# Performance work log

Measured on AMD Instinct MI355X. Metric: run time of the kernel, lower is better.

The kernel has to match this reference:

```python
import jax, jax.numpy as jnp
import numpy as np

SIZE_IN = 4096
SIZE_OUT = 4096
COEF = 8


def _make_mask(size_in, size_out, coef):
    # block-diagonal canceler: output row block i sees input column block i
    inp_sec = size_in // coef
    out_sec = size_out // coef
    row_block = np.arange(size_out) // out_sec  # [size_out]
    col_block = np.arange(size_in) // inp_sec   # [size_in]
    return (row_block[:, None] == col_block[None, :]).astype(np.float32)


def setup_inputs() -> dict:
    key = jax.random.key(0)
    kx, kw, kb = jax.random.split(key, 3)
    x = jax.random.normal(kx, (16384, SIZE_IN), dtype=jnp.float32)
    # kaiming_uniform_(a=sqrt(5)) on [size_out, size_in]: bound = sqrt(6/((1+5)*fan_in)) = 1/sqrt(fan_in)
    bound_w = 1.0 / np.sqrt(SIZE_IN)
    weights = jax.random.uniform(kw, (SIZE_OUT, SIZE_IN), minval=-bound_w, maxval=bound_w, dtype=jnp.float32)
    bound_b = 1.0 / np.sqrt(SIZE_IN)
    bias = jax.random.uniform(kb, (SIZE_OUT,), minval=-bound_b, maxval=bound_b, dtype=jnp.float32)
    mask = jnp.asarray(_make_mask(SIZE_IN, SIZE_OUT, COEF))
    return {"x": x, "weights": weights, "bias": bias, "mask": mask}


def reference(x, weights, bias, mask):
    # faithful to torch: full dense GEMM on the masked weight
    w = weights * mask                      # [size_out, size_in]
    return x @ w.T + bias                   # [batch, size_out]
```

## Files before the change

### kernel.cpp

```cpp
#include <hip/hip_runtime.h>
#include <hip/hip_bf16.h>


typedef __bf16 bf16x8 __attribute__((ext_vector_type(8)));
typedef float  f32x4  __attribute__((ext_vector_type(4)));

constexpr int LD = 4096;

__device__ __forceinline__ bf16x8 cvt8(f32x4 u, f32x4 v) {
    bf16x8 p;
    p[0] = (__bf16)u[0]; p[1] = (__bf16)u[1]; p[2] = (__bf16)u[2]; p[3] = (__bf16)u[3];
    p[4] = (__bf16)v[0]; p[5] = (__bf16)v[1]; p[6] = (__bf16)v[2]; p[7] = (__bf16)v[3];
    return p;
}

__device__ __forceinline__ void gload32(f32x4& q0, f32x4& q1, const void* p) {
    asm volatile("global_load_dwordx4 %0, %2, off\n\t"
                 "global_load_dwordx4 %1, %2, off offset:16"
                 : "=&v"(q0), "=&v"(q1)
                 : "v"(p));
}

__global__ __launch_bounds__(256)
void pack_w(const float* __restrict__ w, __bf16* __restrict__ wt)
{
    const int g = blockIdx.x * 256 + threadIdx.x;
    const int base = g * 16;
    const int o = base >> 9;
    const int k = base & 511;
    const float* src = w + (size_t)o * LD + ((o >> 9) << 9) + k;
    f32x4 a = *(const f32x4*)(src);
    f32x4 b = *(const f32x4*)(src + 4);
    f32x4 c = *(const f32x4*)(src + 8);
    f32x4 d = *(const f32x4*)(src + 12);
    *(bf16x8*)(wt + base)     = cvt8(a, b);
    *(bf16x8*)(wt + base + 8) = cvt8(c, d);
}

__global__ __launch_bounds__(512, 4)
void fc_gemm(const float* __restrict__ x, const __bf16* __restrict__ wt,
             const float* __restrict__ bias, float* __restrict__ out)
{
    __shared__ __align__(16) char smem[81920];

    const int tid  = threadIdx.x;
    const int lane = tid & 63;
    const int wid  = tid >> 6;
    const int wm   = wid >> 2;
    const int wn   = wid & 3;

    const int bid  = blockIdx.x;
    const int xcd  = bid & 7;
    const int slot = bid >> 3;
    const int gm   = slot >> 1;
    const int nh   = slot & 1;
    const int koff = xcd << 9;

    const int trA = tid >> 3;
    const int qA  = tid & 7;
    const int soA = trA * 128 + ((qA * 16) ^ ((trA & 7) << 4));
    const float* xs = x + (size_t)(gm * 64 + trA) * LD + koff + qA * 8;

    const int trB = tid >> 1;
    const int hB  = tid & 1;
    const int swB = (trB & 7) << 4;
    int soB[4];
#pragma unroll
    for (int s = 0; s < 4; ++s)
        soB[s] = trB * 128 + ((hB * 64 + s * 16) ^ swB);
    const __bf16* bs = wt + (size_t)(xcd * 512 + nh * 256 + trB) * 512 + hB * 32;

    f32x4 stA[2][2];
    f32x4 stB[2][2][2];

    f32x4 acc[2][4];
#pragma unroll
    for (int i = 0; i < 2; ++i)
#pragma unroll
        for (int n = 0; n < 4; ++n)
            acc[i][n] = {0.f, 0.f, 0.f, 0.f};

    auto issueTile = [&](int kt, int set) {
        gload32(stB[set][0][0], stB[set][0][1], bs + kt * 64);
        gload32(stB[set][1][0], stB[set][1][1], bs + kt * 64 + 16);
        gload32(stA[set][0], stA[set][1], xs + kt * 64);
    };
    auto storeTile = [&](int set, int buf) {
        char* ab = smem + buf * 8192;
        char* bb = smem + 16384 + buf * 32768;
        *(bf16x8*)(ab + soA) = cvt8(stA[set][0], stA[set][1]);
        *(f32x4*)(bb + soB[0]) = stB[set][0][0];
        *(f32x4*)(bb + soB[1]) = stB[set][0][1];
        *(f32x4*)(bb + soB[2]) = stB[set][1][0];
        *(f32x4*)(bb + soB[3]) = stB[set][1][1];
    };

    issueTile(0, 0);
    issueTile(1, 1);
    asm volatile("s_waitcnt vmcnt(6)" ::: "memory");
    __builtin_amdgcn_sched_barrier(0);
    storeTile(0, 0);
    asm volatile("s_waitcnt lgkmcnt(0)" ::: "memory");
    __builtin_amdgcn_s_barrier();

    const int arow = lane & 15;
    const int ag   = lane >> 4;
    const int fswz = (arow & 7) << 4;
    const int aRowBase = (wm * 32 + arow) * 128;
    const int bRowBase = (wn * 64 + arow) * 128;

#pragma unroll
    for (int kt = 0; kt < 8; ++kt) {
        const int cur = kt & 1;
        if (kt < 6) issueTile(kt + 2, cur);

        const char* aB = smem + cur * 8192;
        const char* bB = smem + 16384 + cur * 32768;
#pragma unroll
        for (int kk = 0; kk < 2; ++kk) {
            const int kx = (kk * 64 + ag * 16) ^ fswz;
            bf16x8 av[2], bv[4];
#pragma unroll
            for (int mf = 0; mf < 2; ++mf)
                av[mf] = *(const bf16x8*)(aB + aRowBase + mf * 2048 + kx);
#pragma unroll
            for (int nf = 0; nf < 4; ++nf)
                bv[nf] = *(const bf16x8*)(bB + bRowBase + nf * 2048 + kx);
#pragma unroll
            for (int mf = 0; mf < 2; ++mf)
#pragma unroll
                for (int nf = 0; nf < 4; ++nf)
                    acc[mf][nf] = __builtin_amdgcn_mfma_f32_16x16x32_bf16(
                        av[mf], bv[nf], acc[mf][nf], 0, 0, 0);
        }

        if (kt < 7) {
            if (kt < 6) { asm volatile("s_waitcnt vmcnt(6)" ::: "memory"); }
            else        { asm volatile("s_waitcnt vmcnt(0)" ::: "memory"); }
            __builtin_amdgcn_sched_barrier(0);
            storeTile(cur ^ 1, cur ^ 1);
            asm volatile("s_waitcnt lgkmcnt(0)" ::: "memory");
            __builtin_amdgcn_s_barrier();
        }
    }

    __syncthreads();

    float* pw = (float*)(smem) + wid * 1280;
    const int r0 = ag * 4;
    const int colbase = xcd * 512 + nh * 256 + wn * 64;
    const int rowg    = gm * 64 + wm * 32;
    float bv4[4];
#pragma unroll
    for (int nf = 0; nf < 4; ++nf)
        bv4[nf] = bias[colbase + nf * 16 + arow];

#pragma unroll
    for (int mf = 0; mf < 2; ++mf) {
#pragma unroll
        for (int nf = 0; nf < 4; ++nf)
#pragma unroll
            for (int r2 = 0; r2 < 4; ++r2) {
                const int lr  = r0 + r2;
                const int col = (nf * 16 + arow) ^ ((lr & 12) << 2);
                pw[lr * 80 + col] = acc[mf][nf][r2] + bv4[nf];
            }
#pragma unroll
        for (int p = 0; p < 4; ++p) {
            const int q  = p * 64 + lane;
            const int lr = q >> 4;
            const int ci = q & 15;
            const f32x4 v4 = *(const f32x4*)(pw + lr * 80 + 4 * (ci ^ (lr & 12)));
            __builtin_nontemporal_store(v4,
                (f32x4*)(out + (size_t)(rowg + mf * 16 + lr) * LD + colbase + ci * 4));
        }
    }
}

extern "C" void kernel_launch(void* const* d_in, const int* in_sizes, int n_in,
                              void* d_out, int out_size, void* d_ws, size_t ws_size,
                              hipStream_t stream)
{
    const float* x    = (const float*)d_in[0];
    const float* wgt  = (const float*)d_in[1];
    const float* bias = (const float*)d_in[2];
    float* out = (float*)d_out;
    __bf16* wt = (__bf16*)d_ws;

    pack_w<<<dim3(512), dim3(256), 0, stream>>>(wgt, wt);
    fc_gemm<<<dim3(4096), dim3(512), 0, stream>>>(x, wt, bias, out);
}
```

Measured before the change: 150.5 us.

## Double M tile to 128 rows and switch to 32x32x16 MFMA

Each block now covers 128 rows of x instead of 64, which halves the grid and the redundant reloads of the packed weight tile per block. The inner loop uses 32x32x16 bf16 MFMA with 64x64 warp tiles instead of 16x16x32 with 32x64, so each LDS fragment read feeds more FLOPs. Shared memory grows to 96KB and the occupancy hint of 4 blocks is dropped, so fewer blocks fit per CU. The epilogue is reworked for the 32x32 accumulator layout.

```diff
diff --git a/kernel.cpp b/kernel.cpp
--- a/kernel.cpp
+++ b/kernel.cpp
@@ -4,6 +4,7 @@
 
 typedef __bf16 bf16x8 __attribute__((ext_vector_type(8)));
 typedef float  f32x4  __attribute__((ext_vector_type(4)));
+typedef float  f32x16 __attribute__((ext_vector_type(16)));
 
 constexpr int LD = 4096;
 
@@ -37,11 +38,11 @@
     *(bf16x8*)(wt + base + 8) = cvt8(c, d);
 }
 
-__global__ __launch_bounds__(512, 4)
+__global__ __launch_bounds__(512)
 void fc_gemm(const float* __restrict__ x, const __bf16* __restrict__ wt,
              const float* __restrict__ bias, float* __restrict__ out)
 {
-    __shared__ __align__(16) char smem[81920];
+    __shared__ __align__(16) char smem[98304];
 
     const int tid  = threadIdx.x;
     const int lane = tid & 63;
@@ -55,11 +56,14 @@
     const int gm   = slot >> 1;
     const int nh   = slot & 1;
     const int koff = xcd << 9;
+    const int colbase = xcd * 512 + nh * 256;
 
-    const int trA = tid >> 3;
-    const int qA  = tid & 7;
-    const int soA = trA * 128 + ((qA * 16) ^ ((trA & 7) << 4));
-    const float* xs = x + (size_t)(gm * 64 + trA) * LD + koff + qA * 8;
+    const int trA = tid >> 2;
+    const int qA  = tid & 3;
+    const int swA = (trA & 7) << 4;
+    const int soA0 = trA * 128 + ((qA * 32)      ^ swA);
+    const int soA1 = trA * 128 + ((qA * 32 + 16) ^ swA);
+    const float* xs = x + (size_t)(gm * 128 + trA) * LD + koff + qA * 16;
 
     const int trB = tid >> 1;
     const int hB  = tid & 1;
@@ -68,74 +72,76 @@
 #pragma unroll
     for (int s = 0; s < 4; ++s)
         soB[s] = trB * 128 + ((hB * 64 + s * 16) ^ swB);
-    const __bf16* bs = wt + (size_t)(xcd * 512 + nh * 256 + trB) * 512 + hB * 32;
+    const __bf16* bs = wt + (size_t)(colbase + trB) * 512 + hB * 32;
 
-    f32x4 stA[2][2];
-    f32x4 stB[2][2][2];
+    f32x4 stA[2][4];
+    f32x4 stB[2][4];
 
-    f32x4 acc[2][4];
+    f32x16 acc[2][2];
 #pragma unroll
     for (int i = 0; i < 2; ++i)
 #pragma unroll
-        for (int n = 0; n < 4; ++n)
-            acc[i][n] = {0.f, 0.f, 0.f, 0.f};
+        for (int n = 0; n < 2; ++n)
+            acc[i][n] = {0.f};
 
     auto issueTile = [&](int kt, int set) {
-        gload32(stB[set][0][0], stB[set][0][1], bs + kt * 64);
-        gload32(stB[set][1][0], stB[set][1][1], bs + kt * 64 + 16);
+        gload32(stB[set][0], stB[set][1], bs + kt * 64);
+        gload32(stB[set][2], stB[set][3], bs + kt * 64 + 16);
         gload32(stA[set][0], stA[set][1], xs + kt * 64);
+        gload32(stA[set][2], stA[set][3], xs + kt * 64 + 8);
     };
     auto storeTile = [&](int set, int buf) {
-        char* ab = smem + buf * 8192;
-        char* bb = smem + 16384 + buf * 32768;
-        *(bf16x8*)(ab + soA) = cvt8(stA[set][0], stA[set][1]);
-        *(f32x4*)(bb + soB[0]) = stB[set][0][0];
-        *(f32x4*)(bb + soB[1]) = stB[set][0][1];
-        *(f32x4*)(bb + soB[2]) = stB[set][1][0];
-        *(f32x4*)(bb + soB[3]) = stB[set][1][1];
+        char* ab = smem + buf * 16384;
+        char* bb = smem + 32768 + buf * 32768;
+        *(bf16x8*)(ab + soA0) = cvt8(stA[set][0], stA[set][1]);
+        *(bf16x8*)(ab + soA1) = cvt8(stA[set][2], stA[set][3]);
+        *(f32x4*)(bb + soB[0]) = stB[set][0];
+        *(f32x4*)(bb + soB[1]) = stB[set][1];
+        *(f32x4*)(bb + soB[2]) = stB[set][2];
+        *(f32x4*)(bb + soB[3]) = stB[set][3];
     };
 
     issueTile(0, 0);
     issueTile(1, 1);
-    asm volatile("s_waitcnt vmcnt(6)" ::: "memory");
+    asm volatile("s_waitcnt vmcnt(8)" ::: "memory");
     __builtin_amdgcn_sched_barrier(0);
     storeTile(0, 0);
     asm volatile("s_waitcnt lgkmcnt(0)" ::: "memory");
     __builtin_amdgcn_s_barrier();
 
-    const int arow = lane & 15;
-    const int ag   = lane >> 4;
-    const int fswz = (arow & 7) << 4;
-    const int aRowBase = (wm * 32 + arow) * 128;
-    const int bRowBase = (wn * 64 + arow) * 128;
+    const int r32 = lane & 31;
+    const int hi  = lane >> 5;
+    const int arow0 = wm * 64 + r32;
+    const int brow0 = wn * 64 + r32;
+    const int aoff0 = arow0 * 128, aoff1 = (arow0 + 32) * 128;
+    const int boff0 = brow0 * 128, boff1 = (brow0 + 32) * 128;
+    const int aswz0 = (arow0 & 7) << 4;
+    const int bswz0 = (brow0 & 7) << 4;
 
 #pragma unroll
     for (int kt = 0; kt < 8; ++kt) {
         const int cur = kt & 1;
         if (kt < 6) issueTile(kt + 2, cur);
 
-        const char* aB = smem + cur * 8192;
-        const char* bB = smem + 16384 + cur * 32768;
+        const char* aB = smem + cur * 16384;
+        const char* bB = smem + 32768 + cur * 32768;
 #pragma unroll
-        for (int kk = 0; kk < 2; ++kk) {
-            const int kx = (kk * 64 + ag * 16) ^ fswz;
-            bf16x8 av[2], bv[4];
-#pragma unroll
-            for (int mf = 0; mf < 2; ++mf)
-                av[mf] = *(const bf16x8*)(aB + aRowBase + mf * 2048 + kx);
-#pragma unroll
-            for (int nf = 0; nf < 4; ++nf)
-                bv[nf] = *(const bf16x8*)(bB + bRowBase + nf * 2048 + kx);
-#pragma unroll
-            for (int mf = 0; mf < 2; ++mf)
-#pragma unroll
-                for (int nf = 0; nf < 4; ++nf)
-                    acc[mf][nf] = __builtin_amdgcn_mfma_f32_16x16x32_bf16(
-                        av[mf], bv[nf], acc[mf][nf], 0, 0, 0);
+        for (int ks = 0; ks < 4; ++ks) {
+            const int ka = (ks * 32 + hi * 16) ^ aswz0;
+            const int kb = (ks * 32 + hi * 16) ^ bswz0;
+            bf16x8 av[2], bv[2];
+            av[0] = *(const bf16x8*)(aB + aoff0 + ka);
+            av[1] = *(const bf16x8*)(aB + aoff1 + ka);
+            bv[0] = *(const bf16x8*)(bB + boff0 + kb);
+            bv[1] = *(const bf16x8*)(bB + boff1 + kb);
+            acc[0][0] = __builtin_amdgcn_mfma_f32_32x32x16_bf16(av[0], bv[0], acc[0][0], 0, 0, 0);
+            acc[0][1] = __builtin_amdgcn_mfma_f32_32x32x16_bf16(av[0], bv[1], acc[0][1], 0, 0, 0);
+            acc[1][0] = __builtin_amdgcn_mfma_f32_32x32x16_bf16(av[1], bv[0], acc[1][0], 0, 0, 0);
+            acc[1][1] = __builtin_amdgcn_mfma_f32_32x32x16_bf16(av[1], bv[1], acc[1][1], 0, 0, 0);
         }
 
         if (kt < 7) {
-            if (kt < 6) { asm volatile("s_waitcnt vmcnt(6)" ::: "memory"); }
+            if (kt < 6) { asm volatile("s_waitcnt vmcnt(8)" ::: "memory"); }
             else        { asm volatile("s_waitcnt vmcnt(0)" ::: "memory"); }
             __builtin_amdgcn_sched_barrier(0);
             storeTile(cur ^ 1, cur ^ 1);
@@ -146,33 +152,31 @@
 
     __syncthreads();
 
-    float* pw = (float*)(smem) + wid * 1280;
-    const int r0 = ag * 4;
-    const int colbase = xcd * 512 + nh * 256 + wn * 64;
-    const int rowg    = gm * 64 + wm * 32;
-    float bv4[4];
+    float* pw = (float*)smem + wid * 2560;
+    float bv2[2];
 #pragma unroll
-    for (int nf = 0; nf < 4; ++nf)
-        bv4[nf] = bias[colbase + nf * 16 + arow];
+    for (int ni = 0; ni < 2; ++ni)
+        bv2[ni] = bias[colbase + wn * 64 + ni * 32 + r32];
 
 #pragma unroll
-    for (int mf = 0; mf < 2; ++mf) {
+    for (int mi = 0; mi < 2; ++mi) {
 #pragma unroll
-        for (int nf = 0; nf < 4; ++nf)
+        for (int ni = 0; ni < 2; ++ni)
 #pragma unroll
-            for (int r2 = 0; r2 < 4; ++r2) {
-                const int lr  = r0 + r2;
-                const int col = (nf * 16 + arow) ^ ((lr & 12) << 2);
-                pw[lr * 80 + col] = acc[mf][nf][r2] + bv4[nf];
+            for (int r = 0; r < 16; ++r) {
+                const int row = (r & 3) + 8 * (r >> 2) + 4 * hi;
+                const int col = (ni * 32 + r32) ^ ((row & 12) << 2);
+                pw[row * 80 + col] = acc[mi][ni][r] + bv2[ni];
             }
 #pragma unroll
-        for (int p = 0; p < 4; ++p) {
+        for (int p = 0; p < 8; ++p) {
             const int q  = p * 64 + lane;
             const int lr = q >> 4;
             const int ci = q & 15;
             const f32x4 v4 = *(const f32x4*)(pw + lr * 80 + 4 * (ci ^ (lr & 12)));
             __builtin_nontemporal_store(v4,
-                (f32x4*)(out + (size_t)(rowg + mf * 16 + lr) * LD + colbase + ci * 4));
+                (f32x4*)(out + (size_t)(gm * 128 + wm * 64 + mi * 32 + lr) * LD
+                         + colbase + wn * 64 + ci * 4));
         }
     }
 }
@@ -188,5 +192,5 @@
     __bf16* wt = (__bf16*)d_ws;
 
     pack_w<<<dim3(512), dim3(256), 0, stream>>>(wgt, wt);
-    fc_gemm<<<dim3(4096), dim3(512), 0, stream>>>(x, wt, bias, out);
+    fc_gemm<<<dim3(2048), dim3(512), 0, stream>>>(x, wt, bias, out);
 }
```

Result: no change. 149.3 us (-0.8%).

## Enlarge GEMM tile to 256x256 with finer-grained interleaved load/MFMA pipeline

Applied to the files above, without the earlier changes.

Each block now computes a 256-row by 256-column output tile instead of 64x256, cutting the grid from 4096 to 1024 blocks. The larger tile lets each loaded weight tile be reused across more rows, reducing redundant global and LDS traffic. The main loop becomes a hand-scheduled ping-pong pipeline where global loads, LDS writes, fragment reads and MFMA bursts are interleaved at half-tile granularity, with barriers and s_setprio around the MFMA groups. In exchange, LDS grows to 128KB and accumulator registers grow fourfold, so occupancy drops to 2 blocks per CU and fewer blocks are available to hide latency.

```diff
diff --git a/kernel.cpp b/kernel.cpp
--- a/kernel.cpp
+++ b/kernel.cpp
@@ -14,11 +14,18 @@
     return p;
 }
 
-__device__ __forceinline__ void gload32(f32x4& q0, f32x4& q1, const void* p) {
+__device__ __forceinline__ void gload64(f32x4& a, f32x4& b, f32x4& c, f32x4& d,
+                                        const void* p) {
+    asm volatile("global_load_dwordx4 %0, %4, off\n\t"
+                 "global_load_dwordx4 %1, %4, off offset:16\n\t"
+                 "global_load_dwordx4 %2, %4, off offset:32\n\t"
+                 "global_load_dwordx4 %3, %4, off offset:48"
+                 : "=&v"(a), "=&v"(b), "=&v"(c), "=&v"(d) : "v"(p));
+}
+__device__ __forceinline__ void gload32(f32x4& a, f32x4& b, const void* p) {
     asm volatile("global_load_dwordx4 %0, %2, off\n\t"
                  "global_load_dwordx4 %1, %2, off offset:16"
-                 : "=&v"(q0), "=&v"(q1)
-                 : "v"(p));
+                 : "=&v"(a), "=&v"(b) : "v"(p));
 }
 
 __global__ __launch_bounds__(256)
@@ -37,11 +44,50 @@
     *(bf16x8*)(wt + base + 8) = cvt8(c, d);
 }
 
-__global__ __launch_bounds__(512, 4)
+#define VMW(N)                                                    \
+    do {                                                          \
+        asm volatile("s_waitcnt vmcnt(" #N ")" ::: "memory");     \
+        __builtin_amdgcn_sched_barrier(0);                        \
+    } while (0)
+
+#define RD(TH, MH, KK)                                                        \
+    do {                                                                      \
+        const char* aB_ = smem + (TH) * 32768;                                \
+        const char* bB_ = smem + 65536 + (TH) * 32768;                        \
+        _Pragma("unroll")                                                     \
+        for (int f = 0; f < 4; ++f) {                                         \
+            const int row = wm * 128 + (MH) * 64 + f * 16 + arow;             \
+            av[f] = *(const bf16x8*)(aB_ + row * 128 +                        \
+                        (((KK) * 64 + ag * 16) ^ ((row & 7) << 4)));          \
+        }                                                                     \
+        _Pragma("unroll")                                                     \
+        for (int n = 0; n < 4; ++n) {                                         \
+            const int row = wn * 64 + n * 16 + arow;                          \
+            bv[n] = *(const bf16x8*)(bB_ + row * 128 +                        \
+                        (((KK) * 64 + ag * 16) ^ ((row & 7) << 4)));          \
+        }                                                                     \
+    } while (0)
+
+#define FIRE(MH)                                                              \
+    do {                                                                      \
+        __builtin_amdgcn_s_barrier();                                         \
+        asm volatile("s_waitcnt lgkmcnt(0)" ::: "memory");                    \
+        __builtin_amdgcn_s_setprio(1);                                        \
+        _Pragma("unroll")                                                     \
+        for (int f = 0; f < 4; ++f)                                           \
+            _Pragma("unroll")                                                 \
+            for (int n = 0; n < 4; ++n)                                       \
+                acc[(MH) * 4 + f][n] = __builtin_amdgcn_mfma_f32_16x16x32_bf16( \
+                    av[f], bv[n], acc[(MH) * 4 + f][n], 0, 0, 0);             \
+        __builtin_amdgcn_s_setprio(0);                                        \
+        __builtin_amdgcn_s_barrier();                                         \
+    } while (0)
+
+__global__ __launch_bounds__(512, 2)
 void fc_gemm(const float* __restrict__ x, const __bf16* __restrict__ wt,
              const float* __restrict__ bias, float* __restrict__ out)
 {
-    __shared__ __align__(16) char smem[81920];
+    __shared__ __align__(16) char smem[131072];
 
     const int tid  = threadIdx.x;
     const int lane = tid & 63;
@@ -50,120 +96,101 @@
     const int wn   = wid & 3;
 
     const int bid  = blockIdx.x;
-    const int xcd  = bid & 7;
+    const int j    = bid & 7;
     const int slot = bid >> 3;
     const int gm   = slot >> 1;
-    const int nh   = slot & 1;
-    const int koff = xcd << 9;
-
-    const int trA = tid >> 3;
-    const int qA  = tid & 7;
-    const int soA = trA * 128 + ((qA * 16) ^ ((trA & 7) << 4));
-    const float* xs = x + (size_t)(gm * 64 + trA) * LD + koff + qA * 8;
-
-    const int trB = tid >> 1;
-    const int hB  = tid & 1;
-    const int swB = (trB & 7) << 4;
-    int soB[4];
-#pragma unroll
-    for (int s = 0; s < 4; ++s)
-        soB[s] = trB * 128 + ((hB * 64 + s * 16) ^ swB);
-    const __bf16* bs = wt + (size_t)(xcd * 512 + nh * 256 + trB) * 512 + hB * 32;
-
-    f32x4 stA[2][2];
-    f32x4 stB[2][2][2];
-
-    f32x4 acc[2][4];
-#pragma unroll
-    for (int i = 0; i < 2; ++i)
+    const int gh   = slot & 1;
+    const int koff    = j << 9;
+    const int colbase = (j << 9) + (gh << 8);
+
+    const int sRow = tid >> 2;
+    const int sQ   = tid & 3;
+    const int swzS = (sRow & 7) << 4;
+    const int soA0 = sRow * 128 + ((sQ * 32)      ^ swzS);
+    const int soA1 = sRow * 128 + ((sQ * 32 + 16) ^ swzS);
+    const float*  xsB = x  + ((size_t)gm * 256 + sRow) * LD + koff + sQ * 16;
+    const __bf16* wtB = wt + ((size_t)colbase + sRow) * 512 + sQ * 16;
+
+    f32x4 stA[2][4];
+    f32x4 stB[2][2];
+
+    f32x4 acc[8][4];
+#pragma unroll
+    for (int i = 0; i < 8; ++i)
 #pragma unroll
         for (int n = 0; n < 4; ++n)
             acc[i][n] = {0.f, 0.f, 0.f, 0.f};
 
-    auto issueTile = [&](int kt, int set) {
-        gload32(stB[set][0][0], stB[set][0][1], bs + kt * 64);
-        gload32(stB[set][1][0], stB[set][1][1], bs + kt * 64 + 16);
-        gload32(stA[set][0], stA[set][1], xs + kt * 64);
-    };
-    auto storeTile = [&](int set, int buf) {
-        char* ab = smem + buf * 8192;
-        char* bb = smem + 16384 + buf * 32768;
-        *(bf16x8*)(ab + soA) = cvt8(stA[set][0], stA[set][1]);
-        *(f32x4*)(bb + soB[0]) = stB[set][0][0];
-        *(f32x4*)(bb + soB[1]) = stB[set][0][1];
-        *(f32x4*)(bb + soB[2]) = stB[set][1][0];
-        *(f32x4*)(bb + soB[3]) = stB[set][1][1];
-    };
-
-    issueTile(0, 0);
-    issueTile(1, 1);
-    asm volatile("s_waitcnt vmcnt(6)" ::: "memory");
-    __builtin_amdgcn_sched_barrier(0);
-    storeTile(0, 0);
+    auto issueA = [&](int kt, int h) {
+        gload64(stA[h][0], stA[h][1], stA[h][2], stA[h][3],
+                xsB + (size_t)h * 128 * LD + kt * 64);
+    };
+    auto issueB = [&](int kt, int h) {
+        gload32(stB[h][0], stB[h][1], wtB + (size_t)h * 65536 + kt * 64);
+    };
+    auto writeA = [&](int kt, int h) {
+        char* base = smem + (kt & 1) * 32768 + h * 16384;
+        *(bf16x8*)(base + soA0) = cvt8(stA[h][0], stA[h][1]);
+        *(bf16x8*)(base + soA1) = cvt8(stA[h][2], stA[h][3]);
+    };
+    auto writeB = [&](int kt, int h) {
+        char* base = smem + 65536 + (kt & 1) * 32768 + h * 16384;
+        *(f32x4*)(base + soA0) = stB[h][0];
+        *(f32x4*)(base + soA1) = stB[h][1];
+    };
+
+    const int arow = lane & 15;
+    const int ag   = lane >> 4;
+    bf16x8 av[4], bv[4];
+
+    issueA(0, 0); issueA(0, 1); issueB(0, 0); issueB(0, 1);
+    VMW(8); writeA(0, 0);
+    VMW(4); writeA(0, 1);
+    VMW(2); writeB(0, 0);
+    VMW(0); writeB(0, 1);
+    issueA(1, 0); issueA(1, 1);
     asm volatile("s_waitcnt lgkmcnt(0)" ::: "memory");
     __builtin_amdgcn_s_barrier();
 
-    const int arow = lane & 15;
-    const int ag   = lane >> 4;
-    const int fswz = (arow & 7) << 4;
-    const int aRowBase = (wm * 32 + arow) * 128;
-    const int bRowBase = (wn * 64 + arow) * 128;
-
-#pragma unroll
-    for (int kt = 0; kt < 8; ++kt) {
-        const int cur = kt & 1;
-        if (kt < 6) issueTile(kt + 2, cur);
-
-        const char* aB = smem + cur * 8192;
-        const char* bB = smem + 16384 + cur * 32768;
-#pragma unroll
-        for (int kk = 0; kk < 2; ++kk) {
-            const int kx = (kk * 64 + ag * 16) ^ fswz;
-            bf16x8 av[2], bv[4];
-#pragma unroll
-            for (int mf = 0; mf < 2; ++mf)
-                av[mf] = *(const bf16x8*)(aB + aRowBase + mf * 2048 + kx);
-#pragma unroll
-            for (int nf = 0; nf < 4; ++nf)
-                bv[nf] = *(const bf16x8*)(bB + bRowBase + nf * 2048 + kx);
-#pragma unroll
-            for (int mf = 0; mf < 2; ++mf)
-#pragma unroll
-                for (int nf = 0; nf < 4; ++nf)
-                    acc[mf][nf] = __builtin_amdgcn_mfma_f32_16x16x32_bf16(
-                        av[mf], bv[nf], acc[mf][nf], 0, 0, 0);
-        }
-
-        if (kt < 7) {
-            if (kt < 6) { asm volatile("s_waitcnt vmcnt(6)" ::: "memory"); }
-            else        { asm volatile("s_waitcnt vmcnt(0)" ::: "memory"); }
-            __builtin_amdgcn_sched_barrier(0);
-            storeTile(cur ^ 1, cur ^ 1);
-            asm volatile("s_waitcnt lgkmcnt(0)" ::: "memory");
-            __builtin_amdgcn_s_barrier();
-        }
+    for (int i = 0; i < 3; ++i) {
+        const int t1 = 2 * i + 1, t2 = 2 * i + 2, t3 = 2 * i + 3;
+        { issueB(t1, 0); RD(0, 0, 0); VMW(6); writeA(t1, 0); FIRE(0); }
+        { issueB(t1, 1); RD(0, 1, 0); VMW(4); writeA(t1, 1); FIRE(1); }
+        { issueA(t2, 0); RD(0, 0, 1); VMW(6); writeB(t1, 0); FIRE(0); }
+        { issueA(t2, 1); RD(0, 1, 1); VMW(8); writeB(t1, 1); FIRE(1); }
+        { issueB(t2, 0); RD(1, 0, 0); VMW(6); writeA(t2, 0); FIRE(0); }
+        { issueB(t2, 1); RD(1, 1, 0); VMW(4); writeA(t2, 1); FIRE(1); }
+        { issueA(t3, 0); RD(1, 0, 1); VMW(6); writeB(t2, 0); FIRE(0); }
+        { issueA(t3, 1); RD(1, 1, 1); VMW(8); writeB(t2, 1); FIRE(1); }
     }
+    { issueB(7, 0); RD(0, 0, 0); VMW(6); writeA(7, 0); FIRE(0); }
+    { issueB(7, 1); RD(0, 1, 0); VMW(4); writeA(7, 1); FIRE(1); }
+    {               RD(0, 0, 1); VMW(2); writeB(7, 0); FIRE(0); }
+    {               RD(0, 1, 1); VMW(0); writeB(7, 1); FIRE(1); }
+    {               RD(1, 0, 0);                        FIRE(0); }
+    {               RD(1, 1, 0);                        FIRE(1); }
+    {               RD(1, 0, 1);                        FIRE(0); }
+    {               RD(1, 1, 1);                        FIRE(1); }
 
     __syncthreads();
 
-    float* pw = (float*)(smem) + wid * 1280;
-    const int r0 = ag * 4;
-    const int colbase = xcd * 512 + nh * 256 + wn * 64;
-    const int rowg    = gm * 64 + wm * 32;
+    float* pw = (float*)smem + wid * 1280;
+    const int colg = colbase + wn * 64;
+    const size_t rowg0 = (size_t)gm * 256 + wm * 128;
     float bv4[4];
 #pragma unroll
-    for (int nf = 0; nf < 4; ++nf)
-        bv4[nf] = bias[colbase + nf * 16 + arow];
-
-#pragma unroll
-    for (int mf = 0; mf < 2; ++mf) {
-#pragma unroll
-        for (int nf = 0; nf < 4; ++nf)
+    for (int n = 0; n < 4; ++n)
+        bv4[n] = bias[colg + n * 16 + arow];
+
+#pragma unroll
+    for (int mi = 0; mi < 8; ++mi) {
+#pragma unroll
+        for (int n = 0; n < 4; ++n)
 #pragma unroll
             for (int r2 = 0; r2 < 4; ++r2) {
-                const int lr  = r0 + r2;
-                const int col = (nf * 16 + arow) ^ ((lr & 12) << 2);
-                pw[lr * 80 + col] = acc[mf][nf][r2] + bv4[nf];
+                const int lr  = ag * 4 + r2;
+                const int col = (n * 16 + arow) ^ ((lr & 12) << 2);
+                pw[lr * 80 + col] = acc[mi][n][r2] + bv4[n];
             }
 #pragma unroll
         for (int p = 0; p < 4; ++p) {
@@ -172,7 +199,7 @@
             const int ci = q & 15;
             const f32x4 v4 = *(const f32x4*)(pw + lr * 80 + 4 * (ci ^ (lr & 12)));
             __builtin_nontemporal_store(v4,
-                (f32x4*)(out + (size_t)(rowg + mf * 16 + lr) * LD + colbase + ci * 4));
+                (f32x4*)(out + (rowg0 + mi * 16 + lr) * LD + colg + ci * 4));
         }
     }
 }
@@ -188,5 +215,5 @@
     __bf16* wt = (__bf16*)d_ws;
 
     pack_w<<<dim3(512), dim3(256), 0, stream>>>(wgt, wt);
-    fc_gemm<<<dim3(4096), dim3(512), 0, stream>>>(x, wt, bias, out);
-}
+    fc_gemm<<<dim3(1024), dim3(512), 0, stream>>>(x, wt, bias, out);
+}
```

New measurement: 131.8 us. 1.14x faster.
